# Kernel tuning notes

Hardware: AMD Instinct MI355X
Metric: run time of the kernel (lower is better)

Reference implementation:

```python
import jax, jax.numpy as jnp
import numpy as np

HID = 2048; NH = 16; DQN = 128; DR = 64; DV = 128; QLR = 1536; KVLR = 512
DQ = DQN + DR  # 192
S = 2048; B = 2
EPS = 1e-6; BASE = 10000.0


def rmsnorm(x, w, eps=EPS):
    xf = x.astype(jnp.float32)
    v = jnp.mean(jnp.square(xf), axis=-1, keepdims=True)
    return (xf * jax.lax.rsqrt(v + eps)).astype(x.dtype) * w


def rope_cos_sin(seq_len, dim):
    inv_freq = 1.0 / (BASE ** (jnp.arange(0, dim, 2, dtype=jnp.float32) / dim))
    freqs = jnp.outer(jnp.arange(seq_len, dtype=jnp.float32), inv_freq)  # [s, d/2]
    emb = jnp.concatenate([freqs, freqs], axis=-1)  # [s, d]
    return jnp.cos(emb), jnp.sin(emb)


def rotate_half(x):
    x1, x2 = jnp.split(x, 2, axis=-1)
    return jnp.concatenate([-x2, x1], axis=-1)


def apply_rope(q, k, cos, sin, position_ids):
    # DeepSeek-V2 variant: interleaved-pair reorder before rotate_half
    cos = cos[position_ids][:, None]  # [b,1,s,d]
    sin = sin[position_ids][:, None]

    def deinterleave(x):
        b, h, s, d = x.shape
        return x.reshape(b, h, s, d // 2, 2).transpose(0, 1, 2, 4, 3).reshape(b, h, s, d)

    q = deinterleave(q)
    k = deinterleave(k)
    return q * cos + rotate_half(q) * sin, k * cos + rotate_half(k) * sin


def setup_inputs() -> dict:
    key = jax.random.key(0)
    ks = jax.random.split(key, 8)
    hidden_states = jax.random.normal(ks[0], (S, B, HID), dtype=jnp.float32)
    causal = jnp.tril(jnp.ones((S, S), dtype=bool))
    attention_mask = jnp.where(causal, 0.0, -1e9).astype(jnp.float32)
    attention_mask = jnp.broadcast_to(attention_mask[None, None], (B, 1, S, S)) + 0.0
    position_ids = jnp.broadcast_to(jnp.arange(S, dtype=jnp.int64 if jax.config.jax_enable_x64 else jnp.int32), (B, S)) + 0
    w = 0.02
    wq_a = jax.random.normal(ks[1], (QLR, HID), dtype=jnp.float32) * w
    q_a_ln_w = jnp.ones((QLR,), dtype=jnp.float32)
    wq_b = jax.random.normal(ks[2], (NH * DQ, QLR), dtype=jnp.float32) * w
    wkv_a = jax.random.normal(ks[3], (KVLR + DR, HID), dtype=jnp.float32) * w
    kv_a_ln_w = jnp.ones((KVLR,), dtype=jnp.float32)
    wkv_b = jax.random.normal(ks[4], (NH * (DQN + DV), KVLR), dtype=jnp.float32) * w
    wo = jax.random.normal(ks[5], (HID, NH * DV), dtype=jnp.float32) * w
    return {"hidden_states": hidden_states, "attention_mask": attention_mask,
            "position_ids": position_ids, "wq_a": wq_a, "q_a_ln_w": q_a_ln_w,
            "wq_b": wq_b, "wkv_a": wkv_a, "kv_a_ln_w": kv_a_ln_w,
            "wkv_b": wkv_b, "wo": wo}


def reference(hidden_states, attention_mask, position_ids, wq_a, q_a_ln_w, wq_b,
              wkv_a, kv_a_ln_w, wkv_b, wo):
    s, b, _ = hidden_states.shape
    # low-rank Q projection: a -> RMSNorm -> b
    q = hidden_states @ wq_a.T                      # [s,b,QLR]
    q = rmsnorm(q, q_a_ln_w) @ wq_b.T               # [s,b,NH*DQ]
    q = q.reshape(s, b, NH, DQ).transpose(1, 2, 0, 3)  # [b,h,s,dq]
    q_nope, q_pe = q[..., :DQN], q[..., DQN:]
    # joint compressed KV + shared rope key
    ckv = hidden_states @ wkv_a.T                   # [s,b,KVLR+DR]
    compressed_kv, k_pe = ckv[..., :KVLR], ckv[..., KVLR:]
    k_pe = k_pe.reshape(s, b, 1, DR).transpose(1, 2, 0, 3)  # [b,1,s,dr]
    kv = rmsnorm(compressed_kv, kv_a_ln_w) @ wkv_b.T         # [s,b,NH*(DQN+DV)]
    kv = kv.reshape(s, b, NH, DQN + DV).transpose(1, 2, 0, 3)
    k_nope, v = kv[..., :DQN], kv[..., DQN:]
    # partial-dim RoPE
    cos, sin = rope_cos_sin(s, DR)
    q_pe, k_pe = apply_rope(q_pe, k_pe, cos, sin, position_ids)
    query = jnp.concatenate([q_nope, q_pe], axis=-1)                 # [b,h,s,dq]
    key = jnp.concatenate([k_nope, jnp.broadcast_to(k_pe, (b, NH, s, DR))], axis=-1)
    scale = DQ ** -0.5
    scores = jnp.einsum('bhqd,bhkd->bhqk', query, key) * scale + attention_mask
    attn = jax.nn.softmax(scores.astype(jnp.float32), axis=-1).astype(query.dtype)
    out = jnp.einsum('bhqk,bhkd->bhqd', attn, v)    # [b,h,s,dv]
    out = out.transpose(2, 0, 1, 3).reshape(s, b, NH * DV)
    return out @ wo.T                               # [s,b,HID]
```

## Files before the change

kernel.cpp:

```cpp
#include <hip/hip_runtime.h>
#include <cmath>

typedef unsigned short u16;
typedef __bf16 bf16x8 __attribute__((ext_vector_type(8)));
typedef float f32x4 __attribute__((ext_vector_type(4)));
typedef unsigned short us8 __attribute__((ext_vector_type(8)));

#define MFMA16(a,b,c) __builtin_amdgcn_mfma_f32_16x16x32_bf16((a),(b),(c),0,0,0)

__device__ __forceinline__ u16 f2bf(float f){
  union { float f; unsigned u; } x; x.f = f;
  unsigned r = x.u + 0x7FFFu + ((x.u >> 16) & 1u);
  return (u16)(r >> 16);
}
__device__ __forceinline__ float bf2f(u16 v){
  union { unsigned u; float f; } x; x.u = ((unsigned)v) << 16; return x.f;
}
__device__ __forceinline__ void gload16(const void* g, void* l){
  __builtin_amdgcn_global_load_lds((const __attribute__((address_space(1))) void*)g,
                                   (__attribute__((address_space(3))) void*)l, 16, 0, 0);
}
__device__ __forceinline__ float block_sum256(float v, float* red, int tid){
  #pragma unroll
  for (int off = 32; off; off >>= 1) v += __shfl_xor(v, off);
  if ((tid & 63) == 0) red[tid >> 6] = v;
  __syncthreads();
  return red[0] + red[1] + red[2] + red[3];
}

__global__ __launch_bounds__(256) void k_convall(const float* __restrict__ s0,
                                                 const float* __restrict__ s1,
                                                 const float* __restrict__ s2,
                                                 const float* __restrict__ s3,
                                                 const float* __restrict__ s4,
                                                 const float* __restrict__ s5,
                                                 u16* __restrict__ d0, u16* __restrict__ d1,
                                                 u16* __restrict__ d2, u16* __restrict__ d3,
                                                 u16* __restrict__ d4, u16* __restrict__ d5){
  const int n0 = 4096 * 2048 / 4;
  const int n1 = 1536 * 2048 / 4;
  const int n2 = 3072 * 1536 / 4;
  const int n3 = 4096 * 512 / 4;
  const int n4 = 2048 * 2048 / 4;
  const int n5 = 640 * 2048 / 4;
  const int total = n0 + n1 + n2 + n3 + n4 + n5;
  const float SCL2 = 0.104117549f;
  int i = blockIdx.x * 256 + threadIdx.x;
  int stride = gridDim.x * 256;
  for (; i < total; i += stride){
    int j = i;
    if (j < n0){
      float4 v = reinterpret_cast<const float4*>(s0)[j];
      ushort4 o; o.x = f2bf(v.x); o.y = f2bf(v.y); o.z = f2bf(v.z); o.w = f2bf(v.w);
      reinterpret_cast<ushort4*>(d0)[j] = o;
    } else if ((j -= n0) < n1){
      float4 v = reinterpret_cast<const float4*>(s1)[j];
      ushort4 o; o.x = f2bf(v.x); o.y = f2bf(v.y); o.z = f2bf(v.z); o.w = f2bf(v.w);
      reinterpret_cast<ushort4*>(d1)[j] = o;
    } else if ((j -= n1) < n2){
      float4 v = reinterpret_cast<const float4*>(s2)[j];
      ushort4 o; o.x = f2bf(v.x * SCL2); o.y = f2bf(v.y * SCL2);
      o.z = f2bf(v.z * SCL2); o.w = f2bf(v.w * SCL2);
      reinterpret_cast<ushort4*>(d2)[j] = o;
    } else if ((j -= n2) < n3){
      float4 v = reinterpret_cast<const float4*>(s3)[j];
      ushort4 o; o.x = f2bf(v.x); o.y = f2bf(v.y); o.z = f2bf(v.z); o.w = f2bf(v.w);
      reinterpret_cast<ushort4*>(d3)[j] = o;
    } else if ((j -= n3) < n4){
      float4 v = reinterpret_cast<const float4*>(s4)[j];
      ushort4 o; o.x = f2bf(v.x); o.y = f2bf(v.y); o.z = f2bf(v.z); o.w = f2bf(v.w);
      reinterpret_cast<ushort4*>(d4)[j] = o;
    } else {
      j -= n4;
      int e = j * 4; int row = e >> 11; int col = e & 2047;
      ushort4 o;
      if (row < 576){
        float4 v = *reinterpret_cast<const float4*>(s5 + (size_t)row * 2048 + col);
        o.x = f2bf(v.x); o.y = f2bf(v.y); o.z = f2bf(v.z); o.w = f2bf(v.w);
      } else { o.x = 0; o.y = 0; o.z = 0; o.w = 0; }
      reinterpret_cast<ushort4*>(d5)[j] = o;
    }
  }
}

template<int OUT_BF16>
__global__ __launch_bounds__(256) void k_gemm(const u16* __restrict__ A,
                                              const u16* __restrict__ Bm,
                                              void* __restrict__ Cv,
                                              int M, int N, int K){
  __shared__ __align__(16) u16 sA[2][128 * 32];
  __shared__ __align__(16) u16 sB[2][128 * 32];
  const int tid = threadIdx.x, w = tid >> 6, l = tid & 63;
  const int ln = l & 15, lg = l >> 4;
  const int id  = blockIdx.x + gridDim.x * blockIdx.y;
  const int nwg = gridDim.x * gridDim.y;
  const int swz = (id & 7) * (nwg >> 3) + (id >> 3);
  const int bx  = swz & (gridDim.x - 1);
  const int by  = swz / gridDim.x;
  const int m0 = bx * 128, n0 = by * 128;
  const int wr = w >> 1, wc = w & 1;
  const int trow = tid >> 2, tcol = (tid & 3) * 8;

  const f32x4 zf = {0.f, 0.f, 0.f, 0.f};
  f32x4 acc[4][4];
  #pragma unroll
  for (int i = 0; i < 4; ++i)
    #pragma unroll
    for (int j = 0; j < 4; ++j) acc[i][j] = zf;

  const u16* ga = A  + (size_t)(m0 + trow) * K + tcol;
  const u16* gb = Bm + (size_t)(n0 + trow) * K + tcol;
  const int nk = K >> 5;

  #define GSTAGE(kt_, bi_) {                                   \
    char* la_ = (char*)sA[bi_] + w * 1024;                     \
    char* lb_ = (char*)sB[bi_] + w * 1024;                     \
    gload16(ga + (kt_) * 32,                  la_);            \
    gload16(ga + (kt_) * 32 + (size_t)64 * K, la_ + 4096);     \
    gload16(gb + (kt_) * 32,                  lb_);            \
    gload16(gb + (kt_) * 32 + (size_t)64 * K, lb_ + 4096);     \
  }

  GSTAGE(0, 0);
  __syncthreads();

  for (int kt = 0; kt < nk; ++kt){
    const int bi = kt & 1;
    if (kt + 1 < nk) GSTAGE(kt + 1, bi ^ 1);

    bf16x8 af[4], bfr[4];
    #pragma unroll
    for (int i = 0; i < 4; ++i)
      af[i] = *(const bf16x8*)&sA[bi][(wr * 64 + i * 16 + ln) * 32 + lg * 8];
    #pragma unroll
    for (int j = 0; j < 4; ++j)
      bfr[j] = *(const bf16x8*)&sB[bi][(wc * 64 + j * 16 + ln) * 32 + lg * 8];
    #pragma unroll
    for (int i = 0; i < 4; ++i)
      #pragma unroll
      for (int j = 0; j < 4; ++j)
        acc[i][j] = MFMA16(af[i], bfr[j], acc[i][j]);

    __syncthreads();
  }
  #undef GSTAGE

  const int mb = m0 + wr * 64, nb = n0 + wc * 64;
  #pragma unroll
  for (int i = 0; i < 4; ++i)
    #pragma unroll
    for (int j = 0; j < 4; ++j)
      #pragma unroll
      for (int r = 0; r < 4; ++r){
        int mm = mb + i * 16 + lg * 4 + r;
        int nn = nb + j * 16 + ln;
        if (OUT_BF16) ((u16*)Cv)[(size_t)mm * N + nn] = f2bf(acc[i][j][r]);
        else          ((float*)Cv)[(size_t)mm * N + nn] = acc[i][j][r];
      }
}

__global__ __launch_bounds__(256) void k_rms_fused(const u16* __restrict__ in,
                                                   const float* __restrict__ wq,
                                                   const float* __restrict__ wkv,
                                                   u16* __restrict__ outq,
                                                   u16* __restrict__ outkv,
                                                   u16* __restrict__ kpe,
                                                   float* __restrict__ cs_tab){
  __shared__ float red[4];
  const int row = blockIdx.x, tid = threadIdx.x;
  const u16* x = in + (size_t)row * 2176;
  float q8[8];
  const bool hasq = tid < 192;
  float ss = 0.f;
  if (hasq){
    us8 v = *(const us8*)(x + tid * 8);
    #pragma unroll
    for (int j = 0; j < 8; ++j){ q8[j] = bf2f(v[j]); ss += q8[j] * q8[j]; }
  }
  float tot = block_sum256(ss, red, tid);
  float inv = rsqrtf(tot * (1.f / 1536.f) + 1e-6f);
  if (hasq){
    union { u16 s[8]; us8 v; } o;
    #pragma unroll
    for (int j = 0; j < 8; ++j) o.s[j] = f2bf(q8[j] * inv * wq[tid * 8 + j]);
    *(us8*)(outq + (size_t)row * 1536 + tid * 8) = o.v;
  }
  __syncthreads();
  float k8[8];
  const bool haskv = tid < 64;
  float ss2 = 0.f;
  if (haskv){
    us8 v = *(const us8*)(x + 1536 + tid * 8);
    #pragma unroll
    for (int j = 0; j < 8; ++j){ k8[j] = bf2f(v[j]); ss2 += k8[j] * k8[j]; }
  }
  float tot2 = block_sum256(ss2, red, tid);
  float inv2 = rsqrtf(tot2 * (1.f / 512.f) + 1e-6f);
  if (haskv){
    union { u16 s[8]; us8 v; } o;
    #pragma unroll
    for (int j = 0; j < 8; ++j) o.s[j] = f2bf(k8[j] * inv2 * wkv[tid * 8 + j]);
    *(us8*)(outkv + (size_t)row * 512 + tid * 8) = o.v;
  }
  if (tid < 32){
    int j = tid;
    float e = bf2f(x[2048 + 2 * j]), o = bf2f(x[2048 + 2 * j + 1]);
    float pos  = (float)(row >> 1);
    float invf = exp2f(-13.287712379549449f * (float)j * (1.f / 32.f));
    float th = pos * invf, sn = sinf(th), cs = cosf(th);
    kpe[(size_t)row * 64 + j]      = f2bf(e * cs - o * sn);
    kpe[(size_t)row * 64 + 32 + j] = f2bf(o * cs + e * sn);
    cs_tab[(size_t)row * 64 + j]      = cs;
    cs_tab[(size_t)row * 64 + 32 + j] = sn;
  }
}

__global__ __launch_bounds__(256) void k_vtrans(const u16* __restrict__ kv,
                                                u16* __restrict__ vt){
  __shared__ u16 t[64][65];
  const int bh = blockIdx.z, b = bh >> 4, h = bh & 15;
  const int s0 = blockIdx.x * 64, d0 = blockIdx.y * 64;
  const int tid = threadIdx.x;
  #pragma unroll
  for (int i = 0; i < 16; ++i){
    int idx = i * 256 + tid; int si = idx >> 6, di = idx & 63;
    t[si][di] = kv[(size_t)((s0 + si) * 2 + b) * 4096 + h * 256 + 128 + d0 + di];
  }
  __syncthreads();
  #pragma unroll
  for (int i = 0; i < 16; ++i){
    int idx = i * 256 + tid; int di = idx >> 6, si = idx & 63;
    vt[(size_t)((b * 16 + h) * 128 + d0 + di) * 2048 + s0 + si] = t[si][di];
  }
}

__global__ __launch_bounds__(256, 2) void k_attn(const u16* __restrict__ q,
                                                 const u16* __restrict__ kv,
                                                 const u16* __restrict__ kpe,
                                                 const u16* __restrict__ vt,
                                                 const float* __restrict__ cs_tab,
                                                 u16* __restrict__ out){
  const int i_ = blockIdx.x + 16 * (blockIdx.y + 16 * blockIdx.z);
  const int j_ = i_ >> 3, x_ = i_ & 7;
  const int g_ = x_ * 4 + (j_ >> 4);
  const int bx = j_ & 15;
  const int h = g_ & 15, b = g_ >> 4;
  const int bh = b * 16 + h;
  const int tid = threadIdx.x, w = tid >> 6, l = tid & 63;
  const int ln = l & 15, lg = l >> 4;

  __shared__ __align__(16) u16 sK[2][64 * 128];
  __shared__ __align__(16) u16 sPE[2][64 * 64];
  __shared__ __align__(16) u16 sV[2][128 * 64];

  const f32x4 zf = {0.f, 0.f, 0.f, 0.f};

  #define PERM(pr_) ((((pr_) >> 5) << 5) + ((((pr_) >> 2) & 3) << 3) + \
                     ((((pr_) >> 4) & 1) << 2) + ((pr_) & 3))
  #define STAGE(kt_, bi_) {                                                     \
    _Pragma("unroll")                                                           \
    for (int p = 0; p < 4; ++p){                                                \
      int o_ = p * 4096 + tid * 16;                                             \
      int pr = o_ >> 8, cl = (o_ >> 4) & 15, cg = cl ^ (pr & 7);                \
      int kl = PERM(pr);                                                        \
      gload16(kv + (size_t)(((kt_) * 64 + kl) * 2 + b) * 4096 + h * 256 + cg * 8, \
              (char*)sK[bi_] + o_);                                             \
    }                                                                           \
    _Pragma("unroll")                                                           \
    for (int p = 0; p < 2; ++p){                                                \
      int o_ = p * 4096 + tid * 16;                                             \
      int pr = o_ >> 7, cl = (o_ >> 4) & 7, cg = cl ^ (pr & 7);                 \
      int kl = PERM(pr);                                                        \
      gload16(kpe + (size_t)(((kt_) * 64 + kl) * 2 + b) * 64 + cg * 8,          \
              (char*)sPE[bi_] + o_);                                            \
    }                                                                           \
    _Pragma("unroll")                                                           \
    for (int p = 0; p < 4; ++p){                                                \
      int o_ = p * 4096 + tid * 16;                                             \
      int row = o_ >> 7, cl = (o_ >> 4) & 7, cg = cl ^ (row & 7);               \
      gload16(vt + (size_t)(bh * 128 + row) * 2048 + (kt_) * 64 + cg * 8,       \
              (char*)sV[bi_] + o_);                                             \
    } }

  for (int half = 0; half < 2; ++half){
    const int qt = half ? (31 - bx) : bx;
    const int qrow0 = qt * 64 + w * 16;
    const int sq = qrow0 + ln;

    bf16x8 qf[6];
    {
      const u16* qr = q + (size_t)(sq * 2 + b) * 3072 + h * 192;
      #pragma unroll
      for (int kb = 0; kb < 4; ++kb) qf[kb] = *(const bf16x8*)(qr + kb * 32 + lg * 8);
      u16 rawa[16];
      *(us8*)&rawa[0] = *(const us8*)(qr + 128 + 16 * lg);
      *(us8*)&rawa[8] = *(const us8*)(qr + 128 + 16 * lg + 8);
      const float* ct = cs_tab + (size_t)(sq * 2 + b) * 64 + 8 * lg;
      float cc[8], ss_[8];
      *(float4*)&cc[0]  = *(const float4*)(ct);
      *(float4*)&cc[4]  = *(const float4*)(ct + 4);
      *(float4*)&ss_[0] = *(const float4*)(ct + 32);
      *(float4*)&ss_[4] = *(const float4*)(ct + 36);
      union { u16 s[8]; bf16x8 v; } pe4, pe5;
      #pragma unroll
      for (int i2 = 0; i2 < 8; ++i2){
        float e  = bf2f(rawa[2 * i2]);
        float o2 = bf2f(rawa[2 * i2 + 1]);
        pe4.s[i2] = f2bf(e * cc[i2] - o2 * ss_[i2]);
        pe5.s[i2] = f2bf(o2 * cc[i2] + e * ss_[i2]);
      }
      qf[4] = pe4.v;
      qf[5] = pe5.v;
    }

    f32x4 o[8];
    float m_i = -3.0e38f, l_i = 0.f;
    #pragma unroll
    for (int c8 = 0; c8 < 8; ++c8) o[c8] = zf;

    const int nkt = qt + 1;
    STAGE(0, 0);
    __syncthreads();

    for (int kt = 0; kt < nkt; ++kt){
      const int bi = kt & 1;
      if (kt + 1 < nkt) STAGE(kt + 1, bi ^ 1);

      f32x4 s_[4];
      #pragma unroll
      for (int cb = 0; cb < 4; ++cb){
        int rl = cb * 16 + ln, swz = rl & 7;
        bf16x8 kf[6];
        #pragma unroll
        for (int kb = 0; kb < 4; ++kb)
          kf[kb] = *(const bf16x8*)((char*)sK[bi] + rl * 256 + (((kb * 4 + lg) ^ swz) << 4));
        kf[4] = *(const bf16x8*)((char*)sPE[bi] + rl * 128 + ((lg ^ swz) << 4));
        kf[5] = *(const bf16x8*)((char*)sPE[bi] + rl * 128 + (((4 + lg) ^ swz) << 4));
        f32x4 acc = zf;
        #pragma unroll
        for (int kb = 0; kb < 6; ++kb)
          acc = MFMA16(kf[kb], qf[kb], acc);
        s_[cb] = acc;
      }

      const bool needMask = (kt * 64 + 63) > qrow0;
      float mx = -3.0e38f;
      #pragma unroll
      for (int cb = 0; cb < 4; ++cb)
        #pragma unroll
        for (int r = 0; r < 4; ++r){
          float v = s_[cb][r];
          if (needMask){
            int sk = kt * 64 + 32 * (cb >> 1) + 8 * lg + 4 * (cb & 1) + r;
            v = (sk <= sq) ? v : -3.0e38f;
          }
          s_[cb][r] = v;
          mx = fmaxf(mx, v);
        }
      mx = fmaxf(mx, __shfl_xor(mx, 16));
      mx = fmaxf(mx, __shfl_xor(mx, 32));
      if (!__all(mx <= m_i + 11.6f)){
        float mn = fmaxf(m_i, mx);
        float sf = exp2f(m_i - mn);
        m_i = mn;
        l_i *= sf;
        float sf0 = __shfl(sf, 4 * lg + 0);
        float sf1 = __shfl(sf, 4 * lg + 1);
        float sf2 = __shfl(sf, 4 * lg + 2);
        float sf3 = __shfl(sf, 4 * lg + 3);
        #pragma unroll
        for (int c8 = 0; c8 < 8; ++c8){
          o[c8][0] *= sf0; o[c8][1] *= sf1; o[c8][2] *= sf2; o[c8][3] *= sf3;
        }
      }
      float rs = 0.f;
      #pragma unroll
      for (int cb = 0; cb < 4; ++cb)
        #pragma unroll
        for (int r = 0; r < 4; ++r){
          float p = exp2f(s_[cb][r] - m_i);
          s_[cb][r] = p;
          rs += p;
        }
      rs += __shfl_xor(rs, 16);
      rs += __shfl_xor(rs, 32);
      l_i += rs;

      bf16x8 pa[2];
      #pragma unroll
      for (int hf = 0; hf < 2; ++hf){
        unsigned pw0, pw1, pw2, pw3;
        f32x4 sa = s_[hf * 2], sb2 = s_[hf * 2 + 1];
        asm("v_cvt_pk_bf16_f32 %0, %1, %2" : "=v"(pw0) : "v"(sa[0]),  "v"(sa[1]));
        asm("v_cvt_pk_bf16_f32 %0, %1, %2" : "=v"(pw1) : "v"(sa[2]),  "v"(sa[3]));
        asm("v_cvt_pk_bf16_f32 %0, %1, %2" : "=v"(pw2) : "v"(sb2[0]), "v"(sb2[1]));
        asm("v_cvt_pk_bf16_f32 %0, %1, %2" : "=v"(pw3) : "v"(sb2[2]), "v"(sb2[3]));
        union { uint4 u; bf16x8 v; } pk;
        pk.u.x = pw0; pk.u.y = pw1; pk.u.z = pw2; pk.u.w = pw3;
        pa[hf] = pk.v;
      }

      #pragma unroll
      for (int c8 = 0; c8 < 8; ++c8){
        int d = c8 * 16 + ln, swz = d & 7;
        bf16x8 vf0 = *(const bf16x8*)((char*)sV[bi] + d * 128 + ((lg ^ swz) << 4));
        bf16x8 vf1 = *(const bf16x8*)((char*)sV[bi] + d * 128 + (((4 + lg) ^ swz) << 4));
        o[c8] = MFMA16(pa[0], vf0, o[c8]);
        o[c8] = MFMA16(pa[1], vf1, o[c8]);
      }
      __syncthreads();
    }

    float li0 = __shfl(l_i, 4 * lg + 0);
    float li1 = __shfl(l_i, 4 * lg + 1);
    float li2 = __shfl(l_i, 4 * lg + 2);
    float li3 = __shfl(l_i, 4 * lg + 3);
    float iv0 = 1.f / li0, iv1 = 1.f / li1, iv2 = 1.f / li2, iv3 = 1.f / li3;
    int sqr = qrow0 + lg * 4;
    #pragma unroll
    for (int c8 = 0; c8 < 8; ++c8){
      int col = h * 128 + c8 * 16 + ln;
      out[(size_t)((sqr + 0) * 2 + b) * 2048 + col] = f2bf(o[c8][0] * iv0);
      out[(size_t)((sqr + 1) * 2 + b) * 2048 + col] = f2bf(o[c8][1] * iv1);
      out[(size_t)((sqr + 2) * 2 + b) * 2048 + col] = f2bf(o[c8][2] * iv2);
      out[(size_t)((sqr + 3) * 2 + b) * 2048 + col] = f2bf(o[c8][3] * iv3);
    }
  }
  #undef STAGE
  #undef PERM
}

extern "C" void kernel_launch(void* const* d_in, const int* in_sizes, int n_in,
                              void* d_out, int out_size, void* d_ws, size_t ws_size,
                              hipStream_t stream){
  const float* hidden    = (const float*)d_in[0];
  const float* wq_a      = (const float*)d_in[3];
  const float* q_a_ln_w  = (const float*)d_in[4];
  const float* wq_b      = (const float*)d_in[5];
  const float* wkv_a     = (const float*)d_in[6];
  const float* kv_a_ln_w = (const float*)d_in[7];
  const float* wkv_b     = (const float*)d_in[8];
  const float* wo        = (const float*)d_in[9];

  char* ws = (char*)d_ws;
  size_t off = 0;
  auto alloc = [&](size_t bytes){ size_t o = off; off += (bytes + 255) & ~(size_t)255; return o; };
  const size_t SB = 4096;

  u16*   hid_bf   = (u16*)(ws + alloc(SB * 2048 * 2));
  u16*   wqab_bf  = (u16*)(ws + alloc((size_t)2176 * 2048 * 2));
  u16*   wqb_bf   = (u16*)(ws + alloc((size_t)3072 * 1536 * 2));
  u16*   wkvb_bf  = (u16*)(ws + alloc((size_t)4096 * 512 * 2));
  u16*   wo_bf    = (u16*)(ws + alloc((size_t)2048 * 2048 * 2));
  u16*   qa_bf    = (u16*)(ws + alloc(SB * 2176 * 2));
  u16*   qrms_bf  = (u16*)(ws + alloc(SB * 1536 * 2));
  u16*   ckvr_bf  = (u16*)(ws + alloc(SB * 512 * 2));
  u16*   kpe_bf   = (u16*)(ws + alloc(SB * 64 * 2));
  float* cs_f     = (float*)(ws + alloc(SB * 64 * 4));
  u16*   qfull_bf = (u16*)(ws + alloc(SB * 3072 * 2));
  u16*   kv_bf    = (u16*)(ws + alloc(SB * 4096 * 2));
  u16*   attn_bf  = (u16*)(ws + alloc(SB * 2048 * 2));
  u16*   vt_bf    = hid_bf;

  dim3 blk(256);
  k_convall<<<2048, blk, 0, stream>>>(hidden, wq_a, wq_b, wkv_b, wo, wkv_a,
                                      hid_bf, wqab_bf, wqb_bf, wkvb_bf, wo_bf,
                                      wqab_bf + (size_t)1536 * 2048);
  k_gemm<1><<<dim3(32, 17), blk, 0, stream>>>(hid_bf, wqab_bf, qa_bf, 4096, 2176, 2048);
  k_rms_fused<<<4096, blk, 0, stream>>>(qa_bf, q_a_ln_w, kv_a_ln_w, qrms_bf, ckvr_bf,
                                        kpe_bf, cs_f);
  k_gemm<1><<<dim3(32, 24), blk, 0, stream>>>(qrms_bf, wqb_bf, qfull_bf, 4096, 3072, 1536);
  k_gemm<1><<<dim3(32, 32), blk, 0, stream>>>(ckvr_bf, wkvb_bf, kv_bf, 4096, 4096, 512);
  k_vtrans<<<dim3(32, 2, 32), blk, 0, stream>>>(kv_bf, vt_bf);
  k_attn<<<dim3(16, 16, 2), blk, 0, stream>>>(qfull_bf, kv_bf, kpe_bf, vt_bf, cs_f, attn_bf);
  k_gemm<0><<<dim3(32, 16), blk, 0, stream>>>(attn_bf, wo_bf, d_out, 4096, 2048, 2048);
}
```

Measured before the change: 301.9 us.

## Merge q_b and kv_b GEMMs into one launch and write transposed V in epilogue

```diff
diff --git a/kernel.cpp b/kernel.cpp
--- a/kernel.cpp
+++ b/kernel.cpp
@@ -159,6 +159,123 @@
       }
 }
 
+__global__ __launch_bounds__(256) void k_gemm23(const u16* __restrict__ A0,
+                                                const u16* __restrict__ B0,
+                                                u16* __restrict__ C0,
+                                                const u16* __restrict__ A1,
+                                                const u16* __restrict__ B1,
+                                                u16* __restrict__ C1,
+                                                u16* __restrict__ Vt){
+  __shared__ __align__(16) u16 lds[16384];
+  char* ldsc = (char*)lds;
+  const int tid = threadIdx.x, w = tid >> 6, l = tid & 63;
+  const int ln = l & 15, lg = l >> 4;
+  const int id  = blockIdx.x + 32 * blockIdx.y;
+  const int nwg = 32 * 56;
+  const int swz = (id & 7) * (nwg >> 3) + (id >> 3);
+  const int bx  = swz & 31;
+  const int by  = swz >> 5;
+  const bool p1 = by >= 24;
+  const u16* A  = p1 ? A1 : A0;
+  const u16* Bm = p1 ? B1 : B0;
+  const int N   = p1 ? 4096 : 3072;
+  const int K   = p1 ? 512  : 1536;
+  const int by_ = p1 ? by - 24 : by;
+  const int m0 = bx * 128, n0 = by_ * 128;
+  const int wr = w >> 1, wc = w & 1;
+  const int trow = tid >> 2, tcol = (tid & 3) * 8;
+
+  const f32x4 zf = {0.f, 0.f, 0.f, 0.f};
+  f32x4 acc[4][4];
+  #pragma unroll
+  for (int i = 0; i < 4; ++i)
+    #pragma unroll
+    for (int j = 0; j < 4; ++j) acc[i][j] = zf;
+
+  const u16* ga = A  + (size_t)(m0 + trow) * K + tcol;
+  const u16* gb = Bm + (size_t)(n0 + trow) * K + tcol;
+  const int nk = K >> 5;
+
+  #define G23STAGE(kt_, bi_) {                                   \
+    char* la_ = ldsc + (bi_) * 8192 + w * 1024;                  \
+    char* lb_ = ldsc + 16384 + (bi_) * 8192 + w * 1024;          \
+    gload16(ga + (kt_) * 32,                  la_);              \
+    gload16(ga + (kt_) * 32 + (size_t)64 * K, la_ + 4096);       \
+    gload16(gb + (kt_) * 32,                  lb_);              \
+    gload16(gb + (kt_) * 32 + (size_t)64 * K, lb_ + 4096);       \
+  }
+
+  G23STAGE(0, 0);
+  __syncthreads();
+
+  for (int kt = 0; kt < nk; ++kt){
+    const int bi = kt & 1;
+    if (kt + 1 < nk) G23STAGE(kt + 1, bi ^ 1);
+
+    bf16x8 af[4], bfr[4];
+    #pragma unroll
+    for (int i = 0; i < 4; ++i)
+      af[i] = *(const bf16x8*)(ldsc + bi * 8192 +
+               (((wr * 64 + i * 16 + ln) * 32 + lg * 8) << 1));
+    #pragma unroll
+    for (int j = 0; j < 4; ++j)
+      bfr[j] = *(const bf16x8*)(ldsc + 16384 + bi * 8192 +
+               (((wc * 64 + j * 16 + ln) * 32 + lg * 8) << 1));
+    #pragma unroll
+    for (int i = 0; i < 4; ++i)
+      #pragma unroll
+      for (int j = 0; j < 4; ++j)
+        acc[i][j] = MFMA16(af[i], bfr[j], acc[i][j]);
+
+    __syncthreads();
+  }
+  #undef G23STAGE
+
+  const bool vtile = p1 && (by_ & 1);
+  if (!vtile){
+    u16* C = p1 ? C1 : C0;
+    const int mb = m0 + wr * 64, nb = n0 + wc * 64;
+    #pragma unroll
+    for (int i = 0; i < 4; ++i)
+      #pragma unroll
+      for (int j = 0; j < 4; ++j)
+        #pragma unroll
+        for (int r = 0; r < 4; ++r){
+          int mm = mb + i * 16 + lg * 4 + r;
+          int nn = nb + j * 16 + ln;
+          C[(size_t)mm * N + nn] = f2bf(acc[i][j][r]);
+        }
+  } else {
+    const int h = by_ >> 1;
+    #pragma unroll
+    for (int i = 0; i < 4; ++i)
+      #pragma unroll
+      for (int j = 0; j < 4; ++j){
+        int nL = wc * 64 + j * 16 + ln;
+        int mL = wr * 64 + i * 16 + lg * 4;
+        union { u16 s[4]; unsigned long long u; } pk4;
+        #pragma unroll
+        for (int r = 0; r < 4; ++r) pk4.s[r] = f2bf(acc[i][j][r]);
+        *(unsigned long long*)(ldsc + nL * 256 + ((mL * 2) ^ ((nL & 7) << 4))) = pk4.u;
+      }
+    __syncthreads();
+    const int s0g = bx * 64;
+    #pragma unroll
+    for (int p = 0; p < 8; ++p){
+      int idx = p * 256 + tid;
+      int d = idx >> 4, mb8 = idx & 15;
+      int m = mb8 * 8;
+      us8 v = *(const us8*)(ldsc + d * 256 + ((m * 2) ^ ((d & 7) << 4)));
+      union { u16 s[4]; unsigned long long u; } e0, e1;
+      e0.s[0] = v[0]; e0.s[1] = v[2]; e0.s[2] = v[4]; e0.s[3] = v[6];
+      e1.s[0] = v[1]; e1.s[1] = v[3]; e1.s[2] = v[5]; e1.s[3] = v[7];
+      int sg = s0g + (m >> 1);
+      *(unsigned long long*)(Vt + ((size_t)(h)      * 128 + d) * 2048 + sg) = e0.u;
+      *(unsigned long long*)(Vt + ((size_t)(16 + h) * 128 + d) * 2048 + sg) = e1.u;
+    }
+  }
+}
+
 __global__ __launch_bounds__(256) void k_rms_fused(const u16* __restrict__ in,
                                                    const float* __restrict__ wq,
                                                    const float* __restrict__ wkv,
@@ -212,25 +329,6 @@
     kpe[(size_t)row * 64 + 32 + j] = f2bf(o * cs + e * sn);
     cs_tab[(size_t)row * 64 + j]      = cs;
     cs_tab[(size_t)row * 64 + 32 + j] = sn;
-  }
-}
-
-__global__ __launch_bounds__(256) void k_vtrans(const u16* __restrict__ kv,
-                                                u16* __restrict__ vt){
-  __shared__ u16 t[64][65];
-  const int bh = blockIdx.z, b = bh >> 4, h = bh & 15;
-  const int s0 = blockIdx.x * 64, d0 = blockIdx.y * 64;
-  const int tid = threadIdx.x;
-  #pragma unroll
-  for (int i = 0; i < 16; ++i){
-    int idx = i * 256 + tid; int si = idx >> 6, di = idx & 63;
-    t[si][di] = kv[(size_t)((s0 + si) * 2 + b) * 4096 + h * 256 + 128 + d0 + di];
-  }
-  __syncthreads();
-  #pragma unroll
-  for (int i = 0; i < 16; ++i){
-    int idx = i * 256 + tid; int di = idx >> 6, si = idx & 63;
-    vt[(size_t)((b * 16 + h) * 128 + d0 + di) * 2048 + s0 + si] = t[si][di];
   }
 }
 
@@ -469,9 +567,8 @@
   k_gemm<1><<<dim3(32, 17), blk, 0, stream>>>(hid_bf, wqab_bf, qa_bf, 4096, 2176, 2048);
   k_rms_fused<<<4096, blk, 0, stream>>>(qa_bf, q_a_ln_w, kv_a_ln_w, qrms_bf, ckvr_bf,
                                         kpe_bf, cs_f);
-  k_gemm<1><<<dim3(32, 24), blk, 0, stream>>>(qrms_bf, wqb_bf, qfull_bf, 4096, 3072, 1536);
-  k_gemm<1><<<dim3(32, 32), blk, 0, stream>>>(ckvr_bf, wkvb_bf, kv_bf, 4096, 4096, 512);
-  k_vtrans<<<dim3(32, 2, 32), blk, 0, stream>>>(kv_bf, vt_bf);
+  k_gemm23<<<dim3(32, 56), blk, 0, stream>>>(qrms_bf, wqb_bf, qfull_bf,
+                                             ckvr_bf, wkvb_bf, kv_bf, vt_bf);
   k_attn<<<dim3(16, 16, 2), blk, 0, stream>>>(qfull_bf, kv_bf, kpe_bf, vt_bf, cs_f, attn_bf);
   k_gemm<0><<<dim3(32, 16), blk, 0, stream>>>(attn_bf, wo_bf, d_out, 4096, 2048, 2048);
 }
```

After: 344.6 us. 1.14x slower.
